# Performance work log

Measured on AMD Instinct MI355X. Metric: run time of the kernel, lower is better.

## Reference

```python
import math
import jax, jax.numpy as jnp
import numpy as np

N, T, C, V = 16, 2048, 512, 500


def setup_inputs() -> dict:
    key = jax.random.key(0)
    k1, k2, k3 = jax.random.split(key, 3)
    x = jax.random.normal(k1, (N, T, C), dtype=jnp.float32)
    x_lens = jax.random.randint(k2, (N,), 1, T + 1).astype(jnp.int64)
    # stand-in for CTC log-posteriors; randn makes the blank channel pass the
    ctc_output = jax.random.normal(k3, (N, T, V), dtype=jnp.float32)
    return {"x": x, "x_lens": x_lens, "ctc_output": ctc_output, "blank_id": 0}


def reference(x, x_lens, ctc_output, blank_id):
    # x: [N, T, C], x_lens: [N], ctc_output: [N, T, V]
    n, t_max, _ = x.shape
    t = jnp.arange(t_max)
    padding_mask = t[None, :] >= x_lens[:, None]                      # [N, T]
    non_blank = (ctc_output[:, :, blank_id] < math.log(0.9)) & (~padding_mask)
    lens_fr = non_blank.sum(axis=1)                                   # [N]
    # stable argsort of ~mask: kept frame indices first, in original order
    order = jnp.argsort(~non_blank, axis=1, stable=True)              # [N, T]
    x_fr = jnp.take_along_axis(x, order[:, :, None], axis=1)          # [N, T, C]
    valid = t[None, :] < lens_fr[:, None]
    x_fr = jnp.where(valid[:, :, None], x_fr, jnp.zeros((), x.dtype))  # zero pad like pad_sequence
    t_prime = int(jnp.max(lens_fr))  # concrete (eager) -> [N, T', C] like torch
    return x_fr[:, :t_prime, :], lens_fr
```

## Files before the change

### kernel.cpp

```cpp
#include <hip/hip_runtime.h>
#include <hip/hip_bf16.h>


__global__ void compact_kernel(const float* __restrict__ ctc,
                               const void* __restrict__ x_lens_raw,
                               const int* __restrict__ blank_id_p,
                               int N, int T, int V,
                               int* __restrict__ idx,
                               int* __restrict__ lens,
                               float* __restrict__ lens_out) {
    const int n   = blockIdx.x;
    const int tid = threadIdx.x;
    const int NTHREADS = 256;
    const int PER = (T + NTHREADS - 1) / NTHREADS;

    const int* li = (const int*)x_lens_raw;
    long long L;
    if (N > 1 && li[1] == 0) {
        L = ((const long long*)x_lens_raw)[n];
    } else {
        L = (long long)li[n];
    }

    const int blank = *blank_id_p;
    const float thr = -0.10536052f;

    unsigned int keepmask = 0u;
    int cnt = 0;
    const int t0 = tid * PER;
    for (int j = 0; j < PER; ++j) {
        int t = t0 + j;
        if (t < T) {
            float v = ctc[((long long)n * T + t) * V + blank];
            bool k = (v < thr) && ((long long)t < L);
            keepmask |= (k ? (1u << j) : 0u);
            cnt += k ? 1 : 0;
        }
    }

    __shared__ int s[NTHREADS];
    s[tid] = cnt;
    __syncthreads();
    if (tid == 0) {
        int acc = 0;
        for (int i = 0; i < NTHREADS; ++i) { int c = s[i]; s[i] = acc; acc += c; }
        lens[n] = acc;
        lens_out[n] = (float)acc;
    }
    __syncthreads();

    int off = s[tid];
    int* my_idx = idx + (long long)n * T;
    for (int j = 0; j < PER; ++j) {
        if (keepmask & (1u << j)) {
            my_idx[off++] = t0 + j;
        }
    }
}

__global__ void gather_kernel(const float* __restrict__ x,
                              const int* __restrict__ idx,
                              const int* __restrict__ lens,
                              float* __restrict__ out,
                              int Tp, int T, int C) {
    const long long row = blockIdx.x;
    const int n = (int)(row / Tp);
    const int p = (int)(row % Tp);
    const int tid = threadIdx.x;

    float4 v = make_float4(0.f, 0.f, 0.f, 0.f);
    if (p < lens[n]) {
        int tsrc = idx[(long long)n * T + p];
        const float4* src = (const float4*)(x + ((long long)n * T + tsrc) * C);
        v = src[tid];
    }
    float4* dst = (float4*)(out + row * (long long)C);
    dst[tid] = v;
}

extern "C" void kernel_launch(void* const* d_in, const int* in_sizes, int n_in,
                              void* d_out, int out_size, void* d_ws, size_t ws_size,
                              hipStream_t stream) {
    const float* x        = (const float*)d_in[0];
    const void*  x_lens   = d_in[1];
    const float* ctc      = (const float*)d_in[2];
    const int*   blank_id = (const int*)d_in[3];

    const int N = in_sizes[1];
    const int C = 512;
    const int V = 500;
    const int T = in_sizes[0] / (N * C);
    const int Tp = (out_size - N) / (N * C);

    int* idx  = (int*)d_ws;
    int* lens = idx + (long long)N * T;

    float* out      = (float*)d_out;
    float* lens_out = out + (long long)N * Tp * C;

    compact_kernel<<<N, 256, 0, stream>>>(ctc, x_lens, blank_id, N, T, V, idx, lens, lens_out);
    gather_kernel<<<(unsigned int)(N * Tp), C / 4, 0, stream>>>(x, idx, lens, out, Tp, T, C);
}
```

Before: 20.91 us.

## Replace per-sample serial compaction with ballot bitmasks and per-row rank search

The old compaction ran one block per sample with a serial prefix scan, which used only 16 blocks. The new mask kernel runs one thread per frame and records 64-bit ballot masks plus popcounts per 64-frame chunk. The gather kernel then rebuilds a chunk prefix in shared memory for each output row and locates the source frame by binary search plus a popcount-based select. This spreads the first stage across the whole GPU, but every gather block now repeats a serial 32-step prefix and its own search. The code also assumes T is a multiple of 256 and 64.

```diff
diff --git a/kernel.cpp b/kernel.cpp
--- a/kernel.cpp
+++ b/kernel.cpp
@@ -2,17 +2,16 @@
 #include <hip/hip_bf16.h>
 
 
-__global__ void compact_kernel(const float* __restrict__ ctc,
-                               const void* __restrict__ x_lens_raw,
-                               const int* __restrict__ blank_id_p,
-                               int N, int T, int V,
-                               int* __restrict__ idx,
-                               int* __restrict__ lens,
-                               float* __restrict__ lens_out) {
-    const int n   = blockIdx.x;
-    const int tid = threadIdx.x;
-    const int NTHREADS = 256;
-    const int PER = (T + NTHREADS - 1) / NTHREADS;
+__global__ void mask_kernel(const float* __restrict__ ctc,
+                            const void* __restrict__ x_lens_raw,
+                            const int* __restrict__ blank_id_p,
+                            int T, int V, int N,
+                            unsigned long long* __restrict__ masks,
+                            int* __restrict__ counts) {
+    const int g = blockIdx.x * 256 + threadIdx.x;
+    const int n = g / T;
+    const int t = g % T;
+    const int lane = threadIdx.x & 63;
 
     const int* li = (const int*)x_lens_raw;
     long long L;
@@ -25,52 +24,57 @@
     const int blank = *blank_id_p;
     const float thr = -0.10536052f;
 
-    unsigned int keepmask = 0u;
-    int cnt = 0;
-    const int t0 = tid * PER;
-    for (int j = 0; j < PER; ++j) {
-        int t = t0 + j;
-        if (t < T) {
-            float v = ctc[((long long)n * T + t) * V + blank];
-            bool k = (v < thr) && ((long long)t < L);
-            keepmask |= (k ? (1u << j) : 0u);
-            cnt += k ? 1 : 0;
-        }
-    }
+    float v = ctc[((long long)n * T + t) * V + blank];
+    bool keep = (v < thr) && ((long long)t < L);
 
-    __shared__ int s[NTHREADS];
-    s[tid] = cnt;
-    __syncthreads();
-    if (tid == 0) {
-        int acc = 0;
-        for (int i = 0; i < NTHREADS; ++i) { int c = s[i]; s[i] = acc; acc += c; }
-        lens[n] = acc;
-        lens_out[n] = (float)acc;
-    }
-    __syncthreads();
-
-    int off = s[tid];
-    int* my_idx = idx + (long long)n * T;
-    for (int j = 0; j < PER; ++j) {
-        if (keepmask & (1u << j)) {
-            my_idx[off++] = t0 + j;
-        }
+    unsigned long long bal = __ballot(keep);
+    if (lane == 0) {
+        int chunk = t >> 6;
+        masks[n * (T >> 6) + chunk] = bal;
+        counts[n * (T >> 6) + chunk] = __popcll(bal);
     }
 }
 
 __global__ void gather_kernel(const float* __restrict__ x,
-                              const int* __restrict__ idx,
-                              const int* __restrict__ lens,
+                              const unsigned long long* __restrict__ masks,
+                              const int* __restrict__ counts,
                               float* __restrict__ out,
+                              float* __restrict__ lens_out,
                               int Tp, int T, int C) {
+    const int NCHUNK = T >> 6;
     const long long row = blockIdx.x;
     const int n = (int)(row / Tp);
     const int p = (int)(row % Tp);
     const int tid = threadIdx.x;
 
+    extern __shared__ int prefix[];
+    if (tid == 0) {
+        int acc = 0;
+        const int* cn = counts + n * NCHUNK;
+        for (int c = 0; c < NCHUNK; ++c) { prefix[c] = acc; acc += cn[c]; }
+        prefix[NCHUNK] = acc;
+    }
+    __syncthreads();
+    const int lens = prefix[NCHUNK];
+
+    if (p == 0 && tid == 0) lens_out[n] = (float)lens;
+
     float4 v = make_float4(0.f, 0.f, 0.f, 0.f);
-    if (p < lens[n]) {
-        int tsrc = idx[(long long)n * T + p];
+    if (p < lens) {
+        int lo = 0, hi = NCHUNK;
+        while (hi - lo > 1) {
+            int mid = (lo + hi) >> 1;
+            if (prefix[mid] <= p) lo = mid; else hi = mid;
+        }
+        int r = p - prefix[lo];
+        unsigned long long m = masks[n * NCHUNK + lo];
+        int base = 0;
+        #pragma unroll
+        for (int w = 32; w >= 1; w >>= 1) {
+            int cnt = __popcll(m & ((1ull << w) - 1ull));
+            if (r >= cnt) { r -= cnt; m >>= w; base += w; }
+        }
+        int tsrc = (lo << 6) + base;
         const float4* src = (const float4*)(x + ((long long)n * T + tsrc) * C);
         v = src[tid];
     }
@@ -91,13 +95,15 @@
     const int V = 500;
     const int T = in_sizes[0] / (N * C);
     const int Tp = (out_size - N) / (N * C);
+    const int NCHUNK = T >> 6;
 
-    int* idx  = (int*)d_ws;
-    int* lens = idx + (long long)N * T;
+    unsigned long long* masks = (unsigned long long*)d_ws;
+    int* counts = (int*)(masks + (long long)N * NCHUNK);
 
     float* out      = (float*)d_out;
     float* lens_out = out + (long long)N * Tp * C;
 
-    compact_kernel<<<N, 256, 0, stream>>>(ctc, x_lens, blank_id, N, T, V, idx, lens, lens_out);
-    gather_kernel<<<(unsigned int)(N * Tp), C / 4, 0, stream>>>(x, idx, lens, out, Tp, T, C);
+    mask_kernel<<<(N * T) / 256, 256, 0, stream>>>(ctc, x_lens, blank_id, T, V, N, masks, counts);
+    gather_kernel<<<(unsigned int)(N * Tp), C / 4, (NCHUNK + 1) * sizeof(int), stream>>>(
+        x, masks, counts, out, lens_out, Tp, T, C);
 }
```

Result: slower. 22.37 us (+7.0%).

## Use wave ballots for stream compaction and flatten the gather grid

Applied to the files above, without the earlier changes.

The compaction kernel now uses 1024 threads per batch row with interleaved frame assignment, so the strided loads of the blank channel are spread across more threads. Per-wave __ballot plus popcount replaces the per-thread bitmask and the 256-entry serial scan, and the serial scan now walks only 32 wave counts. The gather kernel moves from one 128-thread block per output row to a flat grid of 256-thread blocks over float4 elements with shift-based indexing. The ballot array is fixed at 4 entries, so T above 4096 would overflow it.

```diff
diff --git a/kernel.cpp b/kernel.cpp
--- a/kernel.cpp
+++ b/kernel.cpp
@@ -5,14 +5,19 @@
 __global__ void compact_kernel(const float* __restrict__ ctc,
                                const void* __restrict__ x_lens_raw,
                                const int* __restrict__ blank_id_p,
-                               int N, int T, int V,
+                               int T, int V, int N,
                                int* __restrict__ idx,
                                int* __restrict__ lens,
                                float* __restrict__ lens_out) {
-    const int n   = blockIdx.x;
-    const int tid = threadIdx.x;
-    const int NTHREADS = 256;
-    const int PER = (T + NTHREADS - 1) / NTHREADS;
+    const int n    = blockIdx.x;
+    const int tid  = threadIdx.x;
+    const int lane = tid & 63;
+    const int wid  = tid >> 6;
+    const int ITERS = (T + 1023) >> 10;
+    const int NCHUNK = ITERS * 16;
+
+    __shared__ int wcnt[64];
+    __shared__ int pfx[65];
 
     const int* li = (const int*)x_lens_raw;
     long long L;
@@ -25,35 +30,38 @@
     const int blank = *blank_id_p;
     const float thr = -0.10536052f;
 
-    unsigned int keepmask = 0u;
-    int cnt = 0;
-    const int t0 = tid * PER;
-    for (int j = 0; j < PER; ++j) {
-        int t = t0 + j;
+    unsigned long long bal[4];
+    #pragma unroll
+    for (int j = 0; j < 4; ++j) bal[j] = 0ull;
+
+    for (int j = 0; j < ITERS; ++j) {
+        int t = (j << 10) + tid;
+        bool keep = false;
         if (t < T) {
             float v = ctc[((long long)n * T + t) * V + blank];
-            bool k = (v < thr) && ((long long)t < L);
-            keepmask |= (k ? (1u << j) : 0u);
-            cnt += k ? 1 : 0;
+            keep = (v < thr) && ((long long)t < L);
         }
+        bal[j] = __ballot(keep);
+        if (lane == 0) wcnt[j * 16 + wid] = __popcll(bal[j]);
     }
+    __syncthreads();
 
-    __shared__ int s[NTHREADS];
-    s[tid] = cnt;
-    __syncthreads();
     if (tid == 0) {
         int acc = 0;
-        for (int i = 0; i < NTHREADS; ++i) { int c = s[i]; s[i] = acc; acc += c; }
+        for (int c = 0; c < NCHUNK; ++c) { pfx[c] = acc; acc += wcnt[c]; }
+        pfx[NCHUNK] = acc;
         lens[n] = acc;
         lens_out[n] = (float)acc;
     }
     __syncthreads();
 
-    int off = s[tid];
     int* my_idx = idx + (long long)n * T;
-    for (int j = 0; j < PER; ++j) {
-        if (keepmask & (1u << j)) {
-            my_idx[off++] = t0 + j;
+    for (int j = 0; j < ITERS; ++j) {
+        int t = (j << 10) + tid;
+        unsigned long long b = bal[j];
+        if (b & (1ull << lane)) {
+            int rank = __popcll(b & ((1ull << lane) - 1ull));
+            my_idx[pfx[j * 16 + wid] + rank] = t;
         }
     }
 }
@@ -62,20 +70,21 @@
                               const int* __restrict__ idx,
                               const int* __restrict__ lens,
                               float* __restrict__ out,
-                              int Tp, int T, int C) {
-    const long long row = blockIdx.x;
-    const int n = (int)(row / Tp);
-    const int p = (int)(row % Tp);
-    const int tid = threadIdx.x;
+                              int Tp, int T, int cshift, int total_f4) {
+    const int gid = blockIdx.x * blockDim.x + threadIdx.x;
+    if (gid >= total_f4) return;
+    const int row = gid >> cshift;
+    const int c4  = gid & ((1 << cshift) - 1);
+    const int n = row / Tp;
+    const int p = row - n * Tp;
 
     float4 v = make_float4(0.f, 0.f, 0.f, 0.f);
     if (p < lens[n]) {
-        int tsrc = idx[(long long)n * T + p];
-        const float4* src = (const float4*)(x + ((long long)n * T + tsrc) * C);
-        v = src[tid];
+        int tsrc = idx[n * T + p];
+        const float4* src = (const float4*)(x + ((long long)(n * T + tsrc) << (cshift + 2)));
+        v = src[c4];
     }
-    float4* dst = (float4*)(out + row * (long long)C);
-    dst[tid] = v;
+    ((float4*)out)[gid] = v;
 }
 
 extern "C" void kernel_launch(void* const* d_in, const int* in_sizes, int n_in,
@@ -91,6 +100,7 @@
     const int V = 500;
     const int T = in_sizes[0] / (N * C);
     const int Tp = (out_size - N) / (N * C);
+    const int cshift = 7;
 
     int* idx  = (int*)d_ws;
     int* lens = idx + (long long)N * T;
@@ -98,6 +108,10 @@
     float* out      = (float*)d_out;
     float* lens_out = out + (long long)N * Tp * C;
 
-    compact_kernel<<<N, 256, 0, stream>>>(ctc, x_lens, blank_id, N, T, V, idx, lens, lens_out);
-    gather_kernel<<<(unsigned int)(N * Tp), C / 4, 0, stream>>>(x, idx, lens, out, Tp, T, C);
+    compact_kernel<<<N, 1024, 0, stream>>>(ctc, x_lens, blank_id, T, V, N,
+                                           idx, lens, lens_out);
+
+    const int total_f4 = N * Tp * (C / 4);
+    const int blocks = (total_f4 + 255) / 256;
+    gather_kernel<<<blocks, 256, 0, stream>>>(x, idx, lens, out, Tp, T, cshift, total_f4);
 }
```

After: 18.85 us. -9.9%, faster.
